# Performance work log

Hardware: AMD Instinct MI355X
Metric: run time of the kernel (lower is better)

The kernel has to match this reference:

```python
import jax, jax.numpy as jnp
import numpy as np

B, C, H, W = 32, 128, 56, 56
O = 256
KH, KW = 3, 3
SH, SW = 1, 1
PH, PW = 1, 1
T = 6          # num_terms
R = 8          # low_rank
D = C * KH * KW          # 1152
R2 = R * KH * KW         # 72


def setup_inputs() -> dict:
    key = jax.random.key(0)
    ks = jax.random.split(key, 6)
    scale = 0.05
    return {
        "x": jax.random.normal(ks[0], (B, C, H, W), dtype=jnp.float32),
        "S1s": jax.random.normal(ks[1], (T, D, R), dtype=jnp.float32) * scale,
        "U1s": jax.random.normal(ks[2], (T, R, O), dtype=jnp.float32) * scale,
        "U2s": jax.random.normal(ks[3], (T, R2, D), dtype=jnp.float32) * scale,
        "S2s": jax.random.normal(ks[4], (T, R2, O), dtype=jnp.float32) * scale,
        "bias": jax.random.normal(ks[5], (O,), dtype=jnp.float32) * scale,
    }


def _extract_windows(x):
    # im2col: pad then gather strided windows; d flattened in (C, kh, kw) order
    xp = jnp.pad(x, ((0, 0), (0, 0), (PH, PH), (PW, PW)))
    Hp, Wp = xp.shape[2], xp.shape[3]
    Ho = (Hp - KH) // SH + 1
    Wo = (Wp - KW) // SW + 1
    # stack KH*KW shifted views -> [B, C, KH*KW, Ho, Wo]
    patches = jnp.stack(
        [xp[:, :, i:i + SH * Ho:SH, j:j + SW * Wo:SW]
         for i in range(KH) for j in range(KW)],
        axis=2,
    )
    # -> [B, Ho, Wo, C, KH*KW] -> [N, C*KH*KW]
    xw = patches.transpose(0, 3, 4, 1, 2).reshape(B * Ho * Wo, D)
    return xw, Ho, Wo


def reference(x, S1s, U1s, U2s, S2s, bias):
    xw, Ho, Wo = _extract_windows(x)                    # [N, D]
    # term 1: x_windows @ S1s[t] @ U1s[t], averaged over terms
    out1 = jnp.einsum('nd,tdr,tro->no', xw, S1s, U1s, optimize=True) / T + bias
    # term 2: x_windows @ U2s[t].T @ S2s[t], averaged over terms
    out2 = jnp.einsum('nd,tdr,tro->no', xw, jnp.swapaxes(U2s, 1, 2), S2s,
                      optimize=True) / T
    # NOTE: bias is added twice, faithfully matching the original module
    out = (out1 + out2 + bias).reshape(B, Ho, Wo, O).transpose(0, 3, 1, 2)
    return out
```

## Files before the change

kernel.cpp:

```cpp
#include <hip/hip_runtime.h>
#include <hip/hip_bf16.h>

typedef __attribute__((ext_vector_type(8))) short  short8;
typedef __attribute__((ext_vector_type(8))) unsigned short ushort8;
typedef __attribute__((ext_vector_type(4))) unsigned short usv4;
typedef __attribute__((ext_vector_type(4))) float  f32x4;

#define D_DIM 1152
#define O_DIM 256
#define N_TOT 100352
#define K_CAT 480

#define XT_H 58
#define XT_ROW (58 * 128)

__device__ __forceinline__ unsigned short f2bf(float f) {
  __hip_bfloat16 h = __float2bfloat16(f);
  return __builtin_bit_cast(unsigned short, h);
}

#define GLOAD_LDS16(g, l)                                              \
  __builtin_amdgcn_global_load_lds(                                    \
      (const __attribute__((address_space(1))) void*)(g),              \
      (__attribute__((address_space(3))) void*)(l), 16, 0, 0)

__global__ __launch_bounds__(256) void wt_kernel(
    const float* __restrict__ S1s, const float* __restrict__ U1s,
    const float* __restrict__ U2s, const float* __restrict__ S2s,
    unsigned short* __restrict__ Wt) {
  __shared__ float A_lds[32][64];
  __shared__ float B_lds[32][64];

  const int bo = blockIdx.x & 3;
  const int bd = blockIdx.x >> 2;
  const int o0  = bo << 6;
  const int dn0 = bd << 6;
  const int rr  = dn0 >> 7;
  const int c0  = dn0 & 127;

  const int tid = threadIdx.x;
  const int ty = tid >> 4, tx = tid & 15;

  float acc[4][4] = {};

  for (int kc = 0; kc < 15; ++kc) {
#pragma unroll
    for (int e = 0; e < 8; ++e) {
      const int li = e * 256 + tid;
      const int kk = li >> 6;
      const int xx = li & 63;
      const int k  = kc * 32 + kk;
      float av, bv;
      if (k < 48) {
        av = U1s[k * O_DIM + o0 + xx];
        const int d_old = (c0 + xx) * 9 + rr;
        bv = S1s[(size_t)((k >> 3) * D_DIM + d_old) * 8 + (k & 7)];
      } else {
        const int kq = k - 48;
        av = S2s[(size_t)kq * O_DIM + o0 + xx];
        const int d_old = (c0 + xx) * 9 + rr;
        bv = U2s[(size_t)kq * D_DIM + d_old];
      }
      A_lds[kk][xx] = av;
      B_lds[kk][xx] = bv;
    }
    __syncthreads();
#pragma unroll
    for (int kk = 0; kk < 32; ++kk) {
      f32x4 a = *(const f32x4*)&A_lds[kk][ty << 2];
      f32x4 b = *(const f32x4*)&B_lds[kk][tx << 2];
#pragma unroll
      for (int i = 0; i < 4; ++i)
#pragma unroll
        for (int j = 0; j < 4; ++j)
          acc[i][j] += a[i] * b[j];
    }
    __syncthreads();
  }

#pragma unroll
  for (int i = 0; i < 4; ++i) {
    usv4 v;
#pragma unroll
    for (int j = 0; j < 4; ++j) v[j] = f2bf(acc[i][j] * (1.0f / 6.0f));
    *(usv4*)(Wt + (size_t)(o0 + (ty << 2) + i) * D_DIM + dn0 + (tx << 2)) = v;
  }
}

__global__ __launch_bounds__(256) void pad_kernel(const float* __restrict__ x,
                                                  unsigned short* __restrict__ xt) {
  int blk = blockIdx.x;
  int b = blk / XT_H, ih = blk - b * XT_H;
  unsigned short* dst = xt + (size_t)blk * XT_ROW;
  int tid = threadIdx.x;

  if (ih == 0 || ih == XT_H - 1) {
    ushort8 z;
#pragma unroll
    for (int q = 0; q < 8; ++q) z[q] = 0;
    for (int i = tid; i < XT_ROW / 8; i += 256) ((ushort8*)dst)[i] = z;
    return;
  }

  __shared__ unsigned short lds[128 * 58];
  int h = ih - 1;
  const float* xb = x + (size_t)b * 128 * 3136 + (size_t)h * 56;
#pragma unroll 4
  for (int r = 0; r < 28; ++r) {
    int idx = r * 256 + tid;
    int c = idx / 56, w2 = idx - c * 56;
    lds[c * 58 + w2] = f2bf(xb[(size_t)c * 3136 + w2]);
  }
  __syncthreads();
#pragma unroll 4
  for (int r = 0; r < 29; ++r) {
    int idx = r * 256 + tid;
    int iw = idx >> 7, c = idx & 127;
    unsigned short v = 0;
    if (iw >= 1 && iw <= 56) v = lds[c * 58 + (iw - 1)];
    dst[idx] = v;
  }
}

__global__ __launch_bounds__(256) void gemm_kernel(
    const unsigned short* __restrict__ Wt, const unsigned short* __restrict__ xt,
    const float* __restrict__ bias, float* __restrict__ out) {
  __shared__ __align__(1024) unsigned short lds[(128 + 128) * 64];
  unsigned short* A_lds = lds;
  unsigned short* B_lds = lds + 128 * 64;

  int bid   = blockIdx.x;
  int lid   = (bid & 7) * 196 + (bid >> 3);
  int ntile = lid >> 1, otile = lid & 1;
  int n0 = ntile << 7, o0 = otile << 7;

  int tid  = threadIdx.x;
  int w    = tid >> 6;
  int lane = tid & 63;
  int wr = (w >> 1) << 6;
  int wc = (w & 1) << 6;

  const unsigned short* ptrA[4];
  const unsigned short* ptrB[4];
#pragma unroll
  for (int j = 0; j < 4; ++j) {
    int chunk = (w << 2) + j;
    int row   = (chunk << 3) + (lane >> 3);
    ptrA[j] = Wt + (size_t)(o0 + row) * D_DIM + ((lane & 7) << 3);
    int n_g = n0 + row;
    int b   = n_g / 3136;
    int s   = n_g - b * 3136;
    int oh  = s / 56, ow = s - oh * 56;
    ptrB[j] = xt + (((size_t)b * XT_H + oh) * XT_H + ow) * 128 + ((lane & 7) << 3);
  }

  f32x4 acc[4][4] = {};

#pragma unroll
  for (int kt = 0; kt < 18; ++kt) {
    const int rr   = kt >> 1;
    const int kh   = rr / 3, kw = rr - kh * 3;
    const int koff = (kh * XT_H + kw) * 128 + ((kt & 1) << 6);
    const int k0   = kt << 6;
#pragma unroll
    for (int j = 0; j < 4; ++j) {
      const int chunk = (w << 2) + j;
      GLOAD_LDS16(ptrA[j] + k0,   A_lds + chunk * 512);
      GLOAD_LDS16(ptrB[j] + koff, B_lds + chunk * 512);
    }
    __syncthreads();
#pragma unroll
    for (int ks = 0; ks < 2; ++ks) {
      const int kof = (ks << 5) + ((lane >> 4) << 3);
      short8 af[4], bfr[4];
#pragma unroll
      for (int m = 0; m < 4; ++m)
        af[m] = *(const short8*)(A_lds + (wr + m * 16 + (lane & 15)) * 64 + kof);
#pragma unroll
      for (int n = 0; n < 4; ++n)
        bfr[n] = *(const short8*)(B_lds + (wc + n * 16 + (lane & 15)) * 64 + kof);
#pragma unroll
      for (int m = 0; m < 4; ++m)
#pragma unroll
        for (int n = 0; n < 4; ++n)
          acc[m][n] = __builtin_amdgcn_mfma_f32_16x16x32_bf16(af[m], bfr[n], acc[m][n], 0, 0, 0);
    }
    __syncthreads();
  }

  const int lr = (lane >> 4) << 2;
  const int lc = lane & 15;
#pragma unroll
  for (int n = 0; n < 4; ++n) {
    const int ng = n0 + wc + n * 16 + lc;
    const int b  = ng / 3136;
    const int s  = ng - b * 3136;
    float* op = out + (size_t)b * (O_DIM * 3136) + s;
#pragma unroll
    for (int m = 0; m < 4; ++m) {
      const int og = o0 + wr + m * 16 + lr;
#pragma unroll
      for (int r = 0; r < 4; ++r)
        op[(size_t)(og + r) * 3136] = acc[m][n][r] + 2.0f * bias[og + r];
    }
  }
}

extern "C" void kernel_launch(void* const* d_in, const int* in_sizes, int n_in,
                              void* d_out, int out_size, void* d_ws, size_t ws_size,
                              hipStream_t stream) {
  const float* x    = (const float*)d_in[0];
  const float* S1s  = (const float*)d_in[1];
  const float* U1s  = (const float*)d_in[2];
  const float* U2s  = (const float*)d_in[3];
  const float* S2s  = (const float*)d_in[4];
  const float* bias = (const float*)d_in[5];
  float* out = (float*)d_out;

  unsigned short* xt = (unsigned short*)d_ws;
  unsigned short* Wt = (unsigned short*)((char*)d_ws + (size_t)32 * XT_H * XT_ROW * 2);

  pad_kernel<<<dim3(32 * XT_H), dim3(256), 0, stream>>>(x, xt);
  wt_kernel<<<dim3(72), dim3(256), 0, stream>>>(S1s, U1s, U2s, S2s, Wt);
  gemm_kernel<<<dim3(1568), dim3(256), 0, stream>>>(Wt, xt, bias, out);
}
```

Before: 137.1 us.

## Pipeline implicit-GEMM with triple-buffered LDS, larger tiles, and swizzled fragments

Rewrites the main GEMM kernel to use 512-thread blocks on 128x256 output tiles. Global-to-LDS loads are triple-buffered two K-steps ahead and interleaved with MFMA phases using explicit waitcnt, barriers and setprio. An XOR swizzle on the LDS layout is meant to cut bank conflicts on fragment reads. The goal is to hide load latency and cut barrier stalls, at the cost of 144KB of LDS per block, fewer blocks, and fragile manual synchronization.

```diff
diff --git a/kernel.cpp b/kernel.cpp
--- a/kernel.cpp
+++ b/kernel.cpp
@@ -9,8 +9,6 @@
 #define D_DIM 1152
 #define O_DIM 256
 #define N_TOT 100352
-#define K_CAT 480
-
 #define XT_H 58
 #define XT_ROW (58 * 128)
 
@@ -122,86 +120,140 @@
   }
 }
 
-__global__ __launch_bounds__(256) void gemm_kernel(
+__device__ __forceinline__ constexpr int KB_OFF(int kt) {
+  int rr = kt >> 1;
+  return ((rr / 3) * 58 + (rr % 3)) * 128 + (kt & 1) * 64;
+}
+
+#define ST_A(kts, sl2, r) \
+  GLOAD_LDS16(pA[r] + (kts) * 64, smem + (sl2) * 24576 + (r) * 4096 + (w << 9))
+#define ST_B(kts, sl2, r) \
+  GLOAD_LDS16(pB[r] + KB_OFF(kts), smem + (sl2) * 24576 + 8192 + (r) * 4096 + (w << 9))
+
+#define LDS_FRAG(base, row, ks)                                            \
+  (*(const short8*)((const char*)(base) +                                  \
+     ((((row) * 128) + (ks) * 64 + ((lane >> 4) << 4)) ^ ((((row) >> 2) & 1) << 5))))
+
+__global__ __launch_bounds__(512, 2) void gemm_kernel(
     const unsigned short* __restrict__ Wt, const unsigned short* __restrict__ xt,
     const float* __restrict__ bias, float* __restrict__ out) {
-  __shared__ __align__(1024) unsigned short lds[(128 + 128) * 64];
-  unsigned short* A_lds = lds;
-  unsigned short* B_lds = lds + 128 * 64;
-
-  int bid   = blockIdx.x;
-  int lid   = (bid & 7) * 196 + (bid >> 3);
-  int ntile = lid >> 1, otile = lid & 1;
-  int n0 = ntile << 7, o0 = otile << 7;
-
-  int tid  = threadIdx.x;
-  int w    = tid >> 6;
-  int lane = tid & 63;
-  int wr = (w >> 1) << 6;
-  int wc = (w & 1) << 6;
-
-  const unsigned short* ptrA[4];
-  const unsigned short* ptrB[4];
-#pragma unroll
-  for (int j = 0; j < 4; ++j) {
-    int chunk = (w << 2) + j;
-    int row   = (chunk << 3) + (lane >> 3);
-    ptrA[j] = Wt + (size_t)(o0 + row) * D_DIM + ((lane & 7) << 3);
-    int n_g = n0 + row;
-    int b   = n_g / 3136;
-    int s   = n_g - b * 3136;
-    int oh  = s / 56, ow = s - oh * 56;
-    ptrB[j] = xt + (((size_t)b * XT_H + oh) * XT_H + ow) * 128 + ((lane & 7) << 3);
+  __shared__ __align__(1024) unsigned short smem[3 * 24576];
+
+  const int bid   = blockIdx.x;
+  const int lid   = (bid & 7) * 98 + (bid >> 3);
+  const int ntile = lid >> 1, otile = lid & 1;
+  const int n0 = ntile << 8;
+  const int o0 = otile << 7;
+
+  const int tid  = threadIdx.x;
+  const int w    = tid >> 6;
+  const int lane = tid & 63;
+  const int wm   = w >> 2;
+  const int wn   = w & 3;
+
+  const unsigned short* pA[2];
+  const unsigned short* pB[4];
+#pragma unroll
+  for (int r = 0; r < 2; ++r) {
+    const int li  = r * 512 + tid;
+    const int row = li >> 3;
+    const int gs  = (li & 7) ^ (((row >> 2) & 1) << 1);
+    pA[r] = Wt + (size_t)(o0 + row) * D_DIM + gs * 8;
+  }
+#pragma unroll
+  for (int r = 0; r < 4; ++r) {
+    const int li  = r * 512 + tid;
+    const int row = li >> 3;
+    const int gs  = (li & 7) ^ (((row >> 2) & 1) << 1);
+    const int n_g = n0 + row;
+    const int b   = n_g / 3136;
+    const int s   = n_g - b * 3136;
+    const int oh  = s / 56, ow = s - oh * 56;
+    pB[r] = xt + (((size_t)b * XT_H + oh) * XT_H + ow) * 128 + gs * 8;
   }
 
   f32x4 acc[4][4] = {};
 
+  ST_A(0, 0, 0); ST_A(0, 0, 1);
+  ST_B(0, 0, 0); ST_B(0, 0, 1); ST_B(0, 0, 2); ST_B(0, 0, 3);
+  ST_A(1, 1, 0); ST_A(1, 1, 1);
+  ST_B(1, 1, 0); ST_B(1, 1, 1); ST_B(1, 1, 2); ST_B(1, 1, 3);
+  asm volatile("s_waitcnt vmcnt(6)" ::: "memory");
+  __builtin_amdgcn_s_barrier();
+
 #pragma unroll
   for (int kt = 0; kt < 18; ++kt) {
-    const int rr   = kt >> 1;
-    const int kh   = rr / 3, kw = rr - kh * 3;
-    const int koff = (kh * XT_H + kw) * 128 + ((kt & 1) << 6);
-    const int k0   = kt << 6;
-#pragma unroll
-    for (int j = 0; j < 4; ++j) {
-      const int chunk = (w << 2) + j;
-      GLOAD_LDS16(ptrA[j] + k0,   A_lds + chunk * 512);
-      GLOAD_LDS16(ptrB[j] + koff, B_lds + chunk * 512);
-    }
-    __syncthreads();
-#pragma unroll
-    for (int ks = 0; ks < 2; ++ks) {
-      const int kof = (ks << 5) + ((lane >> 4) << 3);
-      short8 af[4], bfr[4];
-#pragma unroll
-      for (int m = 0; m < 4; ++m)
-        af[m] = *(const short8*)(A_lds + (wr + m * 16 + (lane & 15)) * 64 + kof);
-#pragma unroll
-      for (int n = 0; n < 4; ++n)
-        bfr[n] = *(const short8*)(B_lds + (wc + n * 16 + (lane & 15)) * 64 + kof);
-#pragma unroll
-      for (int m = 0; m < 4; ++m)
-#pragma unroll
-        for (int n = 0; n < 4; ++n)
-          acc[m][n] = __builtin_amdgcn_mfma_f32_16x16x32_bf16(af[m], bfr[n], acc[m][n], 0, 0, 0);
-    }
-    __syncthreads();
+    const int sl  = kt % 3;
+    const int kts = kt + 2;
+    const int sl2 = kts % 3;
+    const unsigned short* As = smem + sl * 24576;
+    const unsigned short* Bs = smem + sl * 24576 + 8192;
+
+    short8 af[4][2], bf[2][2], bf2[2][2];
+
+#pragma unroll
+    for (int mi = 0; mi < 4; ++mi) {
+      const int row = (wm << 6) + (mi << 4) + (lane & 15);
+      af[mi][0] = LDS_FRAG(As, row, 0);
+      af[mi][1] = LDS_FRAG(As, row, 1);
+    }
+#pragma unroll
+    for (int ni = 0; ni < 2; ++ni) {
+      const int row = (wn << 6) + (ni << 4) + (lane & 15);
+      bf[ni][0] = LDS_FRAG(Bs, row, 0);
+      bf[ni][1] = LDS_FRAG(Bs, row, 1);
+    }
+    if (kts < 18) { ST_A(kts, sl2, 0); ST_A(kts, sl2, 1); ST_B(kts, sl2, 0); }
+    __builtin_amdgcn_s_barrier();
+    __builtin_amdgcn_s_setprio(1);
+#pragma unroll
+    for (int mi = 0; mi < 4; ++mi)
+#pragma unroll
+      for (int ni = 0; ni < 2; ++ni)
+#pragma unroll
+        for (int ks = 0; ks < 2; ++ks)
+          acc[mi][ni] = __builtin_amdgcn_mfma_f32_16x16x32_bf16(
+              af[mi][ks], bf[ni][ks], acc[mi][ni], 0, 0, 0);
+    __builtin_amdgcn_s_setprio(0);
+    __builtin_amdgcn_s_barrier();
+
+#pragma unroll
+    for (int ni = 0; ni < 2; ++ni) {
+      const int row = (wn << 6) + ((ni + 2) << 4) + (lane & 15);
+      bf2[ni][0] = LDS_FRAG(Bs, row, 0);
+      bf2[ni][1] = LDS_FRAG(Bs, row, 1);
+    }
+    if (kts < 18) { ST_B(kts, sl2, 1); ST_B(kts, sl2, 2); ST_B(kts, sl2, 3); }
+    __builtin_amdgcn_s_barrier();
+    __builtin_amdgcn_s_setprio(1);
+#pragma unroll
+    for (int mi = 0; mi < 4; ++mi)
+#pragma unroll
+      for (int ni = 0; ni < 2; ++ni)
+#pragma unroll
+        for (int ks = 0; ks < 2; ++ks)
+          acc[mi][2 + ni] = __builtin_amdgcn_mfma_f32_16x16x32_bf16(
+              af[mi][ks], bf2[ni][ks], acc[mi][2 + ni], 0, 0, 0);
+    __builtin_amdgcn_s_setprio(0);
+    if (kt < 16) asm volatile("s_waitcnt vmcnt(6)" ::: "memory");
+    else         asm volatile("s_waitcnt vmcnt(0)" ::: "memory");
+    __builtin_amdgcn_s_barrier();
   }
 
   const int lr = (lane >> 4) << 2;
   const int lc = lane & 15;
 #pragma unroll
-  for (int n = 0; n < 4; ++n) {
-    const int ng = n0 + wc + n * 16 + lc;
+  for (int ni = 0; ni < 4; ++ni) {
+    const int ng = n0 + (wn << 6) + (ni << 4) + lc;
     const int b  = ng / 3136;
     const int s  = ng - b * 3136;
     float* op = out + (size_t)b * (O_DIM * 3136) + s;
 #pragma unroll
-    for (int m = 0; m < 4; ++m) {
-      const int og = o0 + wr + m * 16 + lr;
+    for (int mi = 0; mi < 4; ++mi) {
+      const int og = o0 + (wm << 6) + (mi << 4) + lr;
 #pragma unroll
       for (int r = 0; r < 4; ++r)
-        op[(size_t)(og + r) * 3136] = acc[m][n][r] + 2.0f * bias[og + r];
+        op[(size_t)(og + r) * 3136] = acc[mi][ni][r] + 2.0f * bias[og + r];
     }
   }
 }
@@ -216,11 +268,12 @@
   const float* S2s  = (const float*)d_in[4];
   const float* bias = (const float*)d_in[5];
   float* out = (float*)d_out;
+  (void)ws_size;
 
   unsigned short* xt = (unsigned short*)d_ws;
   unsigned short* Wt = (unsigned short*)((char*)d_ws + (size_t)32 * XT_H * XT_ROW * 2);
 
   pad_kernel<<<dim3(32 * XT_H), dim3(256), 0, stream>>>(x, xt);
   wt_kernel<<<dim3(72), dim3(256), 0, stream>>>(S1s, U1s, U2s, S2s, Wt);
-  gemm_kernel<<<dim3(1568), dim3(256), 0, stream>>>(Wt, xt, bias, out);
-}
+  gemm_kernel<<<dim3(784), dim3(512), 0, stream>>>(Wt, xt, bias, out);
+}
```

Result: no change. 138.8 us, median of 2 (+1.2%).
